# Kernel tuning notes

Hardware: AMD Instinct MI355X
Metric: run time of the kernel (lower is better)

## Reference

```python
import jax, jax.numpy as jnp
import numpy as np

C = 64; H = 80; W = 120; B = 2; V = 3; BV = B * V; D = 20
NEAR = 0.1; FAR = 100.0
BF16 = jnp.bfloat16


def conv2d(x, w, b, pad):
    y = jax.lax.conv_general_dilated(x, w, (1, 1), [(pad, pad), (pad, pad)],
                                     dimension_numbers=('NCHW', 'OIHW', 'NCHW'))
    return y + b[None, :, None, None]


def bn2d(x, g, b, m, v, eps=1e-5):
    # BatchNorm2d in inference mode (running stats)
    scale = g / jnp.sqrt(v + eps)
    return (x - m[None, :, None, None]) * scale[None, :, None, None] + b[None, :, None, None]


def grid_sample(feat, grid):
    # feat [N,C,Hf,Wf], grid [N,Hg,Wg,2] in [-1,1]; bilinear, zeros padding, align_corners=True
    _, _, Hf, Wf = feat.shape
    gx = (grid[..., 0] + 1.0) * 0.5 * (Wf - 1)
    gy = (grid[..., 1] + 1.0) * 0.5 * (Hf - 1)
    x0 = jnp.floor(gx); y0 = jnp.floor(gy)

    def one(f, gx, gy, x0, y0):
        def gather(xi, yi):
            valid = (xi >= 0) & (xi < Wf) & (yi >= 0) & (yi < Hf)
            xc = jnp.clip(xi, 0, Wf - 1).astype(jnp.int32)
            yc = jnp.clip(yi, 0, Hf - 1).astype(jnp.int32)
            return f[:, yc, xc] * valid.astype(f.dtype)
        wx = gx - x0; wy = gy - y0
        return (gather(x0, y0) * ((1 - wx) * (1 - wy))
                + gather(x0 + 1, y0) * (wx * (1 - wy))
                + gather(x0, y0 + 1) * ((1 - wx) * wy)
                + gather(x0 + 1, y0 + 1) * (wx * wy))
    return jax.vmap(one)(feat, gx, gy, x0, y0)


def forward(x, intrinsics, c2ws,
            pf_bn1_g, pf_bn1_b, pf_bn1_m, pf_bn1_v, pf_w1, pf_b1,
            pf_bn2_g, pf_bn2_b, pf_bn2_m, pf_bn2_v, pf_w2, pf_b2,
            cp_w, cp_b, cf_bn_g, cf_bn_b, cf_bn_m, cf_bn_v, cf_w, cf_b):
    # ---- flag[0]: predicted depth -> world xyz, position_fusion ----
    depth = 255.0 * (0.5 * jnp.tanh(x[:, 0]) + 0.5)                       # [BV,H,W]
    d16 = depth.astype(BF16)
    ug = jnp.broadcast_to(jnp.arange(W, dtype=jnp.float32)[None, :], (H, W)).astype(BF16)
    vg = jnp.broadcast_to(jnp.arange(H, dtype=jnp.float32)[:, None], (H, W)).astype(BF16)
    cam = jnp.stack([ug[None] * d16, vg[None] * d16, d16], axis=-1).reshape(BV, H * W, 3)
    Kinv = jnp.linalg.inv(intrinsics.astype(jnp.float32)).astype(BF16)
    xyz = jnp.einsum('nij,npj->npi', Kinv, cam)                           # cam coords
    xyz = jnp.einsum('nij,npj->npi', c2ws[:, :3, :3].astype(BF16), xyz) \
          + c2ws[:, :3, 3].astype(BF16)[:, None, :]                       # world coords
    xyz = xyz.reshape(BV, H, W, 3).transpose(0, 3, 1, 2).astype(x.dtype)
    h = jnp.concatenate([xyz, x], axis=1)                                 # [BV,C+3,H,W]
    h = jax.nn.silu(conv2d(bn2d(h, pf_bn1_g, pf_bn1_b, pf_bn1_m, pf_bn1_v), pf_w1, pf_b1, 4))
    h = jax.nn.silu(conv2d(bn2d(h, pf_bn2_g, pf_bn2_b, pf_bn2_m, pf_bn2_v), pf_w2, pf_b2, 4))

    # ---- flag[1]: multi-view plane-sweep correlation ----
    xr = h.reshape(B, V, C, H, W)
    vb = lambda t: t.transpose(1, 0, 2, 3, 4).reshape(BV, C, H, W)        # 'b v ... -> (v b) ...'
    feat01 = vb(xr)
    Ki = intrinsics.reshape(B, V, 3, 3)
    intr_curr = jax.lax.stop_gradient(
        (Ki * jnp.array([W, H, 1.0], jnp.float32)[None, None, :, None]).transpose(1, 0, 2, 3).reshape(BV, 3, 3))
    E = jax.lax.stop_gradient(c2ws.reshape(B, V, 4, 4))
    Einv = jnp.linalg.inv(E)
    dmin, dmax = 1.0 / FAR, 1.0 / NEAR
    depth_vals = 1.0 / (dmin + jnp.linspace(0.0, 1.0, D) * (dmax - dmin))  # [D]
    pix = jnp.stack([jnp.broadcast_to(jnp.arange(W, dtype=jnp.float32)[None, :], (H, W)),
                     jnp.broadcast_to(jnp.arange(H, dtype=jnp.float32)[:, None], (H, W)),
                     jnp.ones((H, W), jnp.float32)], 0).reshape(3, H * W)
    Kinv_c = jnp.linalg.inv(intr_curr).astype(BF16)

    corr = 0.0
    for idx in range(1, V):
        order = list(range(V))[idx:] + list(range(V))[:idx]
        feat10 = vb(xr[:, jnp.array(order)])                              # [BV,C,H,W]
        pose = jnp.concatenate([E[:, o] @ Einv[:, v0] for v0, o in enumerate(order)], axis=0)  # [BV,4,4]
        pts = jnp.einsum('bij,jp->bip', Kinv_c, pix.astype(BF16))
        pts = jnp.einsum('bij,bjp->bip', pose[:, :3, :3].astype(BF16), pts)
        pts = pts[:, :, None, :] * depth_vals.astype(BF16)[None, None, :, None] \
              + pose[:, :3, 3].astype(BF16)[:, :, None, None]             # [BV,3,D,HW]
        pts = jnp.einsum('bij,bjdp->bidp', intr_curr.astype(BF16), pts).astype(jnp.float32)
        den = jnp.maximum(pts[:, 2], 1e-3)
        grid = jnp.stack([2.0 * pts[:, 0] / den / (W - 1) - 1.0,
                          2.0 * pts[:, 1] / den / (H - 1) - 1.0], axis=-1)
        grid = jax.lax.stop_gradient(grid.reshape(BV, D * H, W, 2))
        warped = grid_sample(feat10, grid).reshape(BV, C, D, H, W)
        corr = corr + jnp.einsum('bchw,bcdhw->bdhw', feat01, warped) / (C ** 0.5)
    corr = corr / (V - 1)

    cin = jnp.concatenate([corr, feat01], axis=1)                         # [BV,D+C,H,W]
    cost = conv2d(cin, cp_w, cp_b, 1).reshape(V, B, C, H, W).transpose(1, 0, 2, 3, 4)
    fused = jnp.concatenate([cost, xr], axis=2).reshape(BV, 2 * C, H, W)
    out = jax.nn.silu(conv2d(bn2d(fused, cf_bn_g, cf_bn_b, cf_bn_m, cf_bn_v), cf_w, cf_b, 4))
    return out


def setup_inputs() -> dict:
    key = jax.random.key(0)
    ks = jax.random.split(key, 24)
    def nrm(i, shape, scale=1.0):
        return scale * jax.random.normal(ks[i], shape, jnp.float32)
    def wconv(i, shape):
        fan_in = int(np.prod(shape[1:]))
        return jax.random.normal(ks[i], shape, jnp.float32) / np.sqrt(fan_in)
    x = nrm(0, (BV, C, H, W))
    Kmat = np.tile(np.array([[1.2, 0, 0.5], [0, 1.6, 0.5], [0, 0, 1.0]], np.float32), (BV, 1, 1))
    intrinsics = jnp.asarray(Kmat)
    c2_list = []
    for i in range(BV):
        th = 0.3 * (i % V) - 0.3
        T = np.eye(4, dtype=np.float32)
        T[:3, :3] = np.array([[np.cos(th), 0, np.sin(th)], [0, 1, 0], [-np.sin(th), 0, np.cos(th)]], np.float32)
        T[:3, 3] = [0.5 * (i % V) - 0.5, 0.0, 0.1]
        c2_list.append(T)
    c2ws = jnp.asarray(np.stack(c2_list))
    # first BN sees raw world-xyz channels (magnitude ~1e4), so realistic running var there
    bn1_v = jnp.concatenate([jnp.full((3,), 1e8, jnp.float32), jnp.ones((C,), jnp.float32)])
    return dict(
        x=x, intrinsics=intrinsics, c2ws=c2ws,
        pf_bn1_g=1.0 + 0.1 * nrm(1, (C + 3,)), pf_bn1_b=0.1 * nrm(2, (C + 3,)),
        pf_bn1_m=0.1 * nrm(3, (C + 3,)), pf_bn1_v=bn1_v,
        pf_w1=wconv(4, (C, C + 3, 9, 9)), pf_b1=0.01 * nrm(5, (C,)),
        pf_bn2_g=1.0 + 0.1 * nrm(6, (C,)), pf_bn2_b=0.1 * nrm(7, (C,)),
        pf_bn2_m=0.1 * nrm(8, (C,)), pf_bn2_v=jnp.ones((C,), jnp.float32),
        pf_w2=wconv(9, (C, C, 9, 9)), pf_b2=0.01 * nrm(10, (C,)),
        cp_w=wconv(11, (C, C + D, 3, 3)), cp_b=0.01 * nrm(12, (C,)),
        cf_bn_g=1.0 + 0.1 * nrm(13, (2 * C,)), cf_bn_b=0.1 * nrm(14, (2 * C,)),
        cf_bn_m=0.1 * nrm(15, (2 * C,)), cf_bn_v=jnp.ones((2 * C,), jnp.float32),
        cf_w=wconv(16, (C, 2 * C, 9, 9)), cf_b=0.01 * nrm(17, (C,)))


def reference(x, intrinsics, c2ws,
              pf_bn1_g, pf_bn1_b, pf_bn1_m, pf_bn1_v, pf_w1, pf_b1,
              pf_bn2_g, pf_bn2_b, pf_bn2_m, pf_bn2_v, pf_w2, pf_b2,
              cp_w, cp_b, cf_bn_g, cf_bn_b, cf_bn_m, cf_bn_v, cf_w, cf_b):
    return forward(x, intrinsics, c2ws,
                   pf_bn1_g, pf_bn1_b, pf_bn1_m, pf_bn1_v, pf_w1, pf_b1,
                   pf_bn2_g, pf_bn2_b, pf_bn2_m, pf_bn2_v, pf_w2, pf_b2,
                   cp_w, cp_b, cf_bn_g, cf_bn_b, cf_bn_m, cf_bn_v, cf_w, cf_b)
```

## Files before the change

### kernel.cpp

```cpp
#include <hip/hip_runtime.h>
#include <math.h>

static constexpr int kH  = 80;
static constexpr int kW  = 120;
static constexpr int kHW = kH * kW;
static constexpr int kBV = 6;
static constexpr int kD  = 20;

typedef __attribute__((ext_vector_type(8)))  short bf16x8;
typedef __attribute__((ext_vector_type(16))) float f32x16;
typedef __attribute__((ext_vector_type(4)))  int   i32x4;
typedef __attribute__((ext_vector_type(2)))  int   i32x2;
typedef __attribute__((ext_vector_type(4)))  float float4v;

__device__ __forceinline__ float bf16r(float x) {
  unsigned u = __float_as_uint(x);
  u += 0x7FFFu + ((u >> 16) & 1u);
  return __uint_as_float(u & 0xFFFF0000u);
}
__device__ __forceinline__ unsigned short bf16c(float x) {
  unsigned u = __float_as_uint(x);
  u += 0x7FFFu + ((u >> 16) & 1u);
  return (unsigned short)(u >> 16);
}
__device__ __forceinline__ int pack2(float a, float b) {
  return (int)((unsigned)bf16c(a) | ((unsigned)bf16c(b) << 16));
}
__device__ __forceinline__ float bl(unsigned pk) {
  return __uint_as_float(pk << 16);
}
__device__ __forceinline__ float bh(unsigned pk) {
  return __uint_as_float(pk & 0xFFFF0000u);
}

struct ConstBuf {
  float bn1_s[67], bn1_o[67];
  float bn2_s[64], bn2_o[64];
  float bnf_s[128], bnf_o[128];
  float Kinv[6][9];
  float Rw[6][9];
  float tw[6][3];
  float Kinvc[6][9];
  float intrc[6][9];
  float poseR[2][6][9];
  float poseT[2][6][3];
  float dvals[20];
};

__device__ void inv3x3(const float* A, float* o) {
  float a = A[0], b = A[1], c = A[2];
  float d = A[3], e = A[4], f = A[5];
  float g = A[6], h = A[7], i = A[8];
  float det = a * (e * i - f * h) - b * (d * i - f * g) + c * (d * h - e * g);
  float id = 1.0f / det;
  o[0] = (e * i - f * h) * id;
  o[1] = -(b * i - c * h) * id;
  o[2] = (b * f - c * e) * id;
  o[3] = -(d * i - f * g) * id;
  o[4] = (a * i - c * g) * id;
  o[5] = -(a * f - c * d) * id;
  o[6] = (d * h - e * g) * id;
  o[7] = -(a * h - b * g) * id;
  o[8] = (a * e - b * d) * id;
}

__device__ void inv4x4(const float* A, float* out) {
  float M[4][8];
  for (int r = 0; r < 4; ++r) {
    for (int c = 0; c < 4; ++c) M[r][c] = A[r * 4 + c];
    for (int c = 0; c < 4; ++c) M[r][4 + c] = (r == c) ? 1.0f : 0.0f;
  }
  for (int col = 0; col < 4; ++col) {
    int p = col;
    float best = fabsf(M[col][col]);
    for (int r = col + 1; r < 4; ++r) {
      float v = fabsf(M[r][col]);
      if (v > best) { best = v; p = r; }
    }
    if (p != col)
      for (int c = 0; c < 8; ++c) { float t = M[col][c]; M[col][c] = M[p][c]; M[p][c] = t; }
    float inv = 1.0f / M[col][col];
    for (int c = 0; c < 8; ++c) M[col][c] *= inv;
    for (int r = 0; r < 4; ++r) {
      if (r == col) continue;
      float f = M[r][col];
      for (int c = 0; c < 8; ++c) M[r][c] -= f * M[col][c];
    }
  }
  for (int r = 0; r < 4; ++r)
    for (int c = 0; c < 4; ++c) out[r * 4 + c] = M[r][4 + c];
}

__device__ void mm4(const float* A, const float* B, float* C) {
  for (int r = 0; r < 4; ++r)
    for (int c = 0; c < 4; ++c) {
      float s = 0.0f;
      for (int k = 0; k < 4; ++k) s += A[r * 4 + k] * B[k * 4 + c];
      C[r * 4 + c] = s;
    }
}

__global__ void consts_kernel(const float* __restrict__ intr, const float* __restrict__ c2,
                              const float* g1, const float* b1, const float* m1, const float* v1,
                              const float* g2, const float* b2, const float* m2, const float* v2,
                              const float* gf, const float* bff, const float* mf, const float* vff,
                              ConstBuf* cb) {
  int tid = threadIdx.x;
  for (int c = tid; c < 67; c += 64) {
    float s = g1[c] / sqrtf(v1[c] + 1e-5f);
    cb->bn1_s[c] = s; cb->bn1_o[c] = b1[c] - m1[c] * s;
  }
  for (int c = tid; c < 64; c += 64) {
    float s = g2[c] / sqrtf(v2[c] + 1e-5f);
    cb->bn2_s[c] = s; cb->bn2_o[c] = b2[c] - m2[c] * s;
  }
  for (int c = tid; c < 128; c += 64) {
    float s = gf[c] / sqrtf(vff[c] + 1e-5f);
    cb->bnf_s[c] = s; cb->bnf_o[c] = bff[c] - mf[c] * s;
  }
  if (tid < 20) {
    float l = (1.0f / 19.0f) * (float)tid;
    cb->dvals[tid] = bf16r(1.0f / (0.01f + l * 9.99f));
  }
  __shared__ float Einv_s[6][16];
  if (tid < 6) {
    float Ki[9];
    inv3x3(intr + tid * 9, Ki);
    for (int k = 0; k < 9; ++k) cb->Kinv[tid][k] = bf16r(Ki[k]);
    const float* T = c2 + tid * 16;
    cb->Rw[tid][0] = bf16r(T[0]);  cb->Rw[tid][1] = bf16r(T[1]);  cb->Rw[tid][2] = bf16r(T[2]);
    cb->Rw[tid][3] = bf16r(T[4]);  cb->Rw[tid][4] = bf16r(T[5]);  cb->Rw[tid][5] = bf16r(T[6]);
    cb->Rw[tid][6] = bf16r(T[8]);  cb->Rw[tid][7] = bf16r(T[9]);  cb->Rw[tid][8] = bf16r(T[10]);
    cb->tw[tid][0] = bf16r(T[3]);  cb->tw[tid][1] = bf16r(T[7]);  cb->tw[tid][2] = bf16r(T[11]);
    inv4x4(T, Einv_s[tid]);
    int vj = tid >> 1, bj = tid & 1, ii = bj * 3 + vj;
    const float* Kk = intr + ii * 9;
    float S[9] = {Kk[0] * 120.0f, Kk[1] * 120.0f, Kk[2] * 120.0f,
                  Kk[3] * 80.0f,  Kk[4] * 80.0f,  Kk[5] * 80.0f,
                  Kk[6],          Kk[7],          Kk[8]};
    for (int k = 0; k < 9; ++k) cb->intrc[tid][k] = bf16r(S[k]);
    float Si[9];
    inv3x3(S, Si);
    for (int k = 0; k < 9; ++k) cb->Kinvc[tid][k] = bf16r(Si[k]);
  }
  __syncthreads();
  if (tid < 12) {
    int t = tid / 6, jj = tid % 6;
    int vj = jj >> 1, bj = jj & 1;
    int o = (vj + t + 1) % 3;
    float P[16];
    mm4(c2 + (bj * 3 + o) * 16, Einv_s[bj * 3 + vj], P);
    for (int r = 0; r < 3; ++r) {
      for (int c = 0; c < 3; ++c) cb->poseR[t][jj][r * 3 + c] = bf16r(P[r * 4 + c]);
      cb->poseT[t][jj][r] = bf16r(P[r * 4 + 3]);
    }
  }
}

template <int K, int CINP, int CINR>
__global__ __launch_bounds__(256)
void prep_w(const float* __restrict__ w, unsigned short* __restrict__ Wp) {
  constexpr int NCH = CINP / 32;
  constexpr int NU = K * K * NCH * 256;
  int u = blockIdx.x * 256 + threadIdx.x;
  if (u >= NU) return;
  int slot = u & 255;
  int rest = u >> 8;
  int ci = rest % NCH;
  int kk = rest / NCH;
  int ky = kk / K, kx = kk - ky * K;
  int oc = slot >> 2;
  int gi = (slot & 3) ^ ((oc >> 2) & 3);
  int chb = ci * 32 + gi * 8;
  unsigned short o[8];
#pragma unroll
  for (int e = 0; e < 8; ++e) {
    int ch = chb + e;
    float val = (ch < CINR) ? w[(((size_t)oc * CINR + ch) * K + ky) * K + kx] : 0.0f;
    o[e] = bf16c(val);
  }
  i32x4 pk;
  pk.x = (int)o[0] | ((int)o[1] << 16);
  pk.y = (int)o[2] | ((int)o[3] << 16);
  pk.z = (int)o[4] | ((int)o[5] << 16);
  pk.w = (int)o[6] | ((int)o[7] << 16);
  *(i32x4*)&Wp[(size_t)u * 8] = pk;
}

__global__ __launch_bounds__(256)
void hn_pack(const float* __restrict__ x, const ConstBuf* __restrict__ cb,
             unsigned short* __restrict__ hn_b) {
  int id = blockIdx.x * 256 + threadIdx.x;
  if (id >= kBV * kHW) return;
  int bv = id / kHW, pix = id - bv * kHW;
  int yy = pix / kW, xx = pix - yy * kW;
  float t0 = tanhf(x[(size_t)bv * 64 * kHW + pix]);
  float depth = 255.0f * (0.5f * t0 + 0.5f);
  float dz = bf16r(depth);
  float cx = bf16r((float)xx * dz);
  float cy = bf16r((float)yy * dz);
  const float* Ki = cb->Kinv[bv];
  float p0 = bf16r(Ki[0] * cx + Ki[1] * cy + Ki[2] * dz);
  float p1 = bf16r(Ki[3] * cx + Ki[4] * cy + Ki[5] * dz);
  float p2 = bf16r(Ki[6] * cx + Ki[7] * cy + Ki[8] * dz);
  const float* R = cb->Rw[bv];
  const float* tw = cb->tw[bv];
  float q[3];
  q[0] = bf16r(bf16r(R[0] * p0 + R[1] * p1 + R[2] * p2) + tw[0]);
  q[1] = bf16r(bf16r(R[3] * p0 + R[4] * p1 + R[5] * p2) + tw[1]);
  q[2] = bf16r(bf16r(R[6] * p0 + R[7] * p1 + R[8] * p2) + tw[2]);
  unsigned short* o = &hn_b[(size_t)id * 96];
  const float* xb = x + (size_t)bv * 64 * kHW + pix;
#pragma unroll
  for (int g = 0; g < 24; ++g) {
    float vv[4];
#pragma unroll
    for (int e = 0; e < 4; ++e) {
      int ch = g * 4 + e;
      float val;
      if (ch < 3) val = q[ch] * cb->bn1_s[ch] + cb->bn1_o[ch];
      else if (ch < 67) val = xb[(size_t)(ch - 3) * kHW] * cb->bn1_s[ch] + cb->bn1_o[ch];
      else val = 0.0f;
      vv[e] = val;
    }
    i32x2 pk = {pack2(vv[0], vv[1]), pack2(vv[2], vv[3])};
    *(i32x2*)(o + g * 4) = pk;
  }
}

template <int CINP, int K, int OUT>
__global__ __launch_bounds__(256)
void conv_mfma(const unsigned short* __restrict__ in_b,
               const unsigned short* __restrict__ Wp,
               const float* __restrict__ bias,
               const ConstBuf* __restrict__ cb,
               float* __restrict__ outf,
               unsigned short* __restrict__ outb,
               unsigned short* __restrict__ outb2) {
  constexpr int NCH = CINP / 32;
  constexpr int KK = K * K;
  constexpr int GN = KK / 3;
  constexpr int PAD = K / 2;
  constexpr int NC = 16 + K - 1;
  constexpr int NR = 16 + K - 1;
  constexpr int NPX = NC * NR;
  __shared__ unsigned short sA[NPX * 32];
  __shared__ unsigned short sB[2][3 * 2048];

  const int tid = threadIdx.x;
  const int w = tid >> 6, l = tid & 63;
  const int bx = blockIdx.x, by = blockIdx.y, bz = blockIdx.z;
  const size_t inbase = (size_t)bz * kHW;

  const int r = l & 31, h = l >> 5;
  const int xloc = r & 15;
  const int rhi = r >> 4;
  f32x16 acc[2][2] = {};

  int boff[2][2];
#pragma unroll
  for (int nt = 0; nt < 2; ++nt)
#pragma unroll
    for (int kc = 0; kc < 2; ++kc) {
      int oc = nt * 32 + (l & 31);
      int gi = kc * 2 + h;
      boff[nt][kc] = (oc * 4 + (gi ^ ((oc >> 2) & 3))) * 8;
    }

  for (int ci = 0; ci < NCH; ++ci) {
    for (int g2 = tid; g2 < NPX * 4; g2 += 256) {
      int px = g2 >> 2, gi = g2 & 3;
      int hy = px / NC, hx = px - hy * NC;
      int gy = by * 16 - PAD + hy, gx = bx * 16 - PAD + hx;
      bool ok = ((unsigned)gy < (unsigned)kH) && ((unsigned)gx < (unsigned)kW);
      i32x4 v = {0, 0, 0, 0};
      if (ok) v = *(const i32x4*)&in_b[(inbase + gy * kW + gx) * CINP + ci * 32 + gi * 8];
      *(i32x4*)&sA[px * 32 + ((gi ^ ((px >> 2) & 3)) << 3)] = v;
    }
#pragma unroll
    for (int t = 0; t < 3; ++t) {
      int u = tid + t * 256;
      int kki = u >> 8, slot = u & 255;
      *(i32x4*)&sB[0][u * 8] =
          *(const i32x4*)&Wp[(((size_t)kki * NCH + ci) * 256 + slot) * 8];
    }
    __syncthreads();

    for (int g = 0; g < GN; ++g) {
      const int cur = g & 1, nxt = cur ^ 1;
      const bool hasnext = (g + 1 < GN);
      i32x4 pf[3];
      if (hasnext) {
#pragma unroll
        for (int t = 0; t < 3; ++t) {
          int u = tid + t * 256;
          int kki = u >> 8, slot = u & 255;
          pf[t] = *(const i32x4*)
              &Wp[(((size_t)((g + 1) * 3 + kki) * NCH + ci) * 256 + slot) * 8];
        }
      }
#pragma unroll
      for (int kki = 0; kki < 3; ++kki) {
        const int kk = g * 3 + kki;
        const int ky = kk / K, kx = kk - ky * K;
        bf16x8 a[2][2];
#pragma unroll
        for (int m = 0; m < 2; ++m) {
          const int hp = (4 * w + 2 * m + rhi + ky) * NC + (xloc + kx);
#pragma unroll
          for (int kc = 0; kc < 2; ++kc) {
            int gi = kc * 2 + h;
            a[m][kc] = *(const bf16x8*)&sA[hp * 32 + ((gi ^ ((hp >> 2) & 3)) << 3)];
          }
        }
        bf16x8 bb[2][2];
#pragma unroll
        for (int nt = 0; nt < 2; ++nt)
#pragma unroll
          for (int kc = 0; kc < 2; ++kc)
            bb[nt][kc] = *(const bf16x8*)&sB[cur][kki * 2048 + boff[nt][kc]];
#pragma unroll
        for (int m = 0; m < 2; ++m)
#pragma unroll
          for (int nt = 0; nt < 2; ++nt) {
            acc[m][nt] = __builtin_amdgcn_mfma_f32_32x32x16_bf16(a[m][0], bb[nt][0], acc[m][nt], 0, 0, 0);
            acc[m][nt] = __builtin_amdgcn_mfma_f32_32x32x16_bf16(a[m][1], bb[nt][1], acc[m][nt], 0, 0, 0);
          }
      }
      if (hasnext) {
#pragma unroll
        for (int t = 0; t < 3; ++t)
          *(i32x4*)&sB[nxt][(tid + t * 256) * 8] = pf[t];
      }
      __syncthreads();
    }
  }

#pragma unroll
  for (int m = 0; m < 2; ++m) {
#pragma unroll
    for (int nt = 0; nt < 2; ++nt) {
      const int oc = nt * 32 + (l & 31);
      const float bs = bias[oc];
      float s2 = 0.f, o2 = 0.f;
      if (OUT == 0) { s2 = cb->bn2_s[oc]; o2 = cb->bn2_o[oc]; }
      if (OUT == 1) { s2 = cb->bnf_s[64 + oc]; o2 = cb->bnf_o[64 + oc]; }
      if (OUT == 2) { s2 = cb->bnf_s[oc]; o2 = cb->bnf_o[oc]; }
#pragma unroll
      for (int reg = 0; reg < 16; ++reg) {
        int row = (reg & 3) + 8 * (reg >> 2) + 4 * h;
        int x = bx * 16 + (row & 15);
        if (x >= kW) continue;
        int y = by * 16 + 4 * w + 2 * m + (row >> 4);
        float v = acc[m][nt][reg] + bs;
        if (OUT != 2) v = v / (1.0f + expf(-v));
        if (OUT == 0) {
          size_t px = inbase + y * kW + x;
          outb[px * 64 + oc] = bf16c(v * s2 + o2);
        } else if (OUT == 1) {
          size_t px = inbase + y * kW + x;
          outb[px * 64 + oc] = bf16c(v);
          outb2[px * 128 + 64 + oc] = bf16c(v * s2 + o2);
        } else if (OUT == 2) {
          int i = (bz & 1) * 3 + (bz >> 1);
          size_t px = (size_t)i * kHW + y * kW + x;
          outb[px * 128 + oc] = bf16c(v * s2 + o2);
        } else {
          outf[((size_t)bz * 64 + oc) * kHW + y * kW + x] = v;
        }
      }
    }
  }
}

__global__ __launch_bounds__(256)
void corr_kernel(const unsigned short* __restrict__ h_b, const ConstBuf* __restrict__ cb,
                 unsigned short* __restrict__ cin_b) {
  __shared__ float sgeo[4][2][40][8];
  const int tid = threadIdx.x;
  const int w = tid >> 6, lane = tid & 63;
  const int pair = blockIdx.x * 4 + w;
  const int j = pair / (kHW / 2);
  const int pix = (pair - j * (kHW / 2)) * 2;
  const int b = j & 1, v = j >> 1;
  const int ph = lane >> 5, cl = lane & 31;
  const int pixl = pix + ph;
  const int dst = b * 3 + v;
  const unsigned f01pk =
      ((const unsigned*)(h_b + ((size_t)dst * kHW + pixl) * 64))[cl];
  const float f01lo = bl(f01pk), f01hi = bh(f01pk);
  const char* sb0 = (const char*)(h_b + (size_t)(b * 3 + ((v + 1) % 3)) * kHW * 64);
  const char* sb1 = (const char*)(h_b + (size_t)(b * 3 + ((v + 2) % 3)) * kHW * 64);

  for (int job = lane; job < 80; job += 64) {
    const int p = job / 40, jj = job - p * 40;
    const int d = jj >> 1, t = jj & 1;
    const int pp = pix + p;
    const int yyp = pp / kW, xxp = pp - yyp * kW;
    const float* Kc = cb->Kinvc[j];
    const float* IC = cb->intrc[j];
    const float uf = (float)xxp, vf = (float)yyp;
    float p1_0 = bf16r(Kc[0] * uf + Kc[1] * vf + Kc[2]);
    float p1_1 = bf16r(Kc[3] * uf + Kc[4] * vf + Kc[5]);
    float p1_2 = bf16r(Kc[6] * uf + Kc[7] * vf + Kc[8]);
    const float* PR = cb->poseR[t][j];
    const float* PT = cb->poseT[t][j];
    float p20 = bf16r(PR[0] * p1_0 + PR[1] * p1_1 + PR[2] * p1_2);
    float p21 = bf16r(PR[3] * p1_0 + PR[4] * p1_1 + PR[5] * p1_2);
    float p22 = bf16r(PR[6] * p1_0 + PR[7] * p1_1 + PR[8] * p1_2);
    float dv = cb->dvals[d];
    float q0 = bf16r(bf16r(p20 * dv) + PT[0]);
    float q1 = bf16r(bf16r(p21 * dv) + PT[1]);
    float q2 = bf16r(bf16r(p22 * dv) + PT[2]);
    float s0 = bf16r(IC[0] * q0 + IC[1] * q1 + IC[2] * q2);
    float s1 = bf16r(IC[3] * q0 + IC[4] * q1 + IC[5] * q2);
    float s2 = bf16r(IC[6] * q0 + IC[7] * q1 + IC[8] * q2);
    float den = fmaxf(s2, 1e-3f);
    float g0 = 2.0f * s0 / den / 119.0f - 1.0f;
    float g1 = 2.0f * s1 / den / 79.0f - 1.0f;
    float gx = (g0 + 1.0f) * 0.5f * 119.0f;
    float gy = (g1 + 1.0f) * 0.5f * 79.0f;
    float x0f = floorf(gx), y0f = floorf(gy);
    float wx = gx - x0f, wy = gy - y0f;
    float x1f = x0f + 1.0f, y1f = y0f + 1.0f;
    float vx0 = (x0f >= 0.0f && x0f < 120.0f) ? 1.0f : 0.0f;
    float vx1 = (x1f >= 0.0f && x1f < 120.0f) ? 1.0f : 0.0f;
    float vy0 = (y0f >= 0.0f && y0f < 80.0f) ? 1.0f : 0.0f;
    float vy1 = (y1f >= 0.0f && y1f < 80.0f) ? 1.0f : 0.0f;
    int xi0 = (int)fminf(fmaxf(x0f, 0.0f), 119.0f);
    int xi1 = (int)fminf(fmaxf(x1f, 0.0f), 119.0f);
    int yi0 = (int)fminf(fmaxf(y0f, 0.0f), 79.0f);
    int yi1 = (int)fminf(fmaxf(y1f, 0.0f), 79.0f);
    int r0b = yi0 * (kW * 128), r1b = yi1 * (kW * 128);
    int c0b = xi0 * 128, c1b = xi1 * 128;
    float* gp = sgeo[w][p][jj];
    gp[0] = __int_as_float(r0b + c0b);
    gp[1] = __int_as_float(r0b + c1b);
    gp[2] = __int_as_float(r1b + c0b);
    gp[3] = __int_as_float(r1b + c1b);
    gp[4] = ((1.0f - wx) * (1.0f - wy)) * (vx0 * vy0);
    gp[5] = (wx * (1.0f - wy)) * (vx1 * vy0);
    gp[6] = ((1.0f - wx) * wy) * (vx0 * vy1);
    gp[7] = (wx * wy) * (vx1 * vy1);
  }
  __syncthreads();

  unsigned short* op = &cin_b[(size_t)(j * kHW + pixl) * 96];
  *(unsigned*)(op + 20 + 2 * cl) = f01pk;
  if (cl < 6) *(unsigned*)(op + 84 + 2 * cl) = 0u;

  const unsigned cl4 = (unsigned)cl * 4u;
#pragma unroll 2
  for (int d = 0; d < kD; ++d) {
    float a = 0.0f;
#pragma unroll
    for (int t = 0; t < 2; ++t) {
      const char* sb = t ? sb1 : sb0;
      const float* gp = sgeo[w][ph][d * 2 + t];
      float4v ga = *(const float4v*)gp;
      float4v gb = *(const float4v*)(gp + 4);
      unsigned k00 = *(const unsigned*)(sb + ((unsigned)__float_as_int(ga.x) + cl4));
      unsigned k10 = *(const unsigned*)(sb + ((unsigned)__float_as_int(ga.y) + cl4));
      unsigned k01 = *(const unsigned*)(sb + ((unsigned)__float_as_int(ga.z) + cl4));
      unsigned k11 = *(const unsigned*)(sb + ((unsigned)__float_as_int(ga.w) + cl4));
      float al = gb.x * bl(k00) + gb.y * bl(k10) + gb.z * bl(k01) + gb.w * bl(k11);
      float ah = gb.x * bh(k00) + gb.y * bh(k10) + gb.z * bh(k01) + gb.w * bh(k11);
      a += al * f01lo + ah * f01hi;
    }
#pragma unroll
    for (int off = 16; off > 0; off >>= 1) a += __shfl_xor(a, off, 64);
    if (cl == 0) op[d] = bf16c(a * 0.0625f);
  }
}

extern "C" void kernel_launch(void* const* d_in, const int* in_sizes, int n_in,
                              void* d_out, int out_size, void* d_ws, size_t ws_size,
                              hipStream_t stream) {
  (void)in_sizes; (void)n_in; (void)out_size; (void)ws_size;
  const float* x    = (const float*)d_in[0];
  const float* intr = (const float*)d_in[1];
  const float* c2w  = (const float*)d_in[2];
  const float* bn1g = (const float*)d_in[3];
  const float* bn1b = (const float*)d_in[4];
  const float* bn1m = (const float*)d_in[5];
  const float* bn1v = (const float*)d_in[6];
  const float* w1   = (const float*)d_in[7];
  const float* b1   = (const float*)d_in[8];
  const float* bn2g = (const float*)d_in[9];
  const float* bn2b = (const float*)d_in[10];
  const float* bn2m = (const float*)d_in[11];
  const float* bn2v = (const float*)d_in[12];
  const float* w2   = (const float*)d_in[13];
  const float* b2   = (const float*)d_in[14];
  const float* cpw  = (const float*)d_in[15];
  const float* cpb  = (const float*)d_in[16];
  const float* bnfg = (const float*)d_in[17];
  const float* bnfb = (const float*)d_in[18];
  const float* bnfm = (const float*)d_in[19];
  const float* bnfv = (const float*)d_in[20];
  const float* wf   = (const float*)d_in[21];
  const float* bff  = (const float*)d_in[22];

  char* ws = (char*)d_ws;
  ConstBuf* cb            = (ConstBuf*)ws;
  unsigned short* hn_b    = (unsigned short*)(ws + 8192);
  unsigned short* h1_b    = (unsigned short*)(ws + 11067392);
  unsigned short* h_b     = (unsigned short*)(ws + 18440192);
  unsigned short* cin_b   = (unsigned short*)(ws + 33185792);
  unsigned short* fused_b = (unsigned short*)(ws + 44244992);
  unsigned short* Wp1     = (unsigned short*)(ws + 58990592);
  unsigned short* Wp2     = (unsigned short*)(ws + 59985920);
  unsigned short* Wpc     = (unsigned short*)(ws + 60649472);
  unsigned short* Wpf     = (unsigned short*)(ws + 60760064);

  consts_kernel<<<1, 64, 0, stream>>>(intr, c2w, bn1g, bn1b, bn1m, bn1v,
                                      bn2g, bn2b, bn2m, bn2v, bnfg, bnfb, bnfm, bnfv, cb);
  prep_w<9, 96, 67><<<243, 256, 0, stream>>>(w1, Wp1);
  prep_w<9, 64, 64><<<162, 256, 0, stream>>>(w2, Wp2);
  prep_w<3, 96, 84><<<27, 256, 0, stream>>>(cpw, Wpc);
  prep_w<9, 128, 128><<<324, 256, 0, stream>>>(wf, Wpf);
  hn_pack<<<225, 256, 0, stream>>>(x, cb, hn_b);

  dim3 cgrid(8, 5, 6);
  conv_mfma<96, 9, 0><<<cgrid, 256, 0, stream>>>(hn_b, Wp1, b1, cb, nullptr, h1_b, nullptr);
  conv_mfma<64, 9, 1><<<cgrid, 256, 0, stream>>>(h1_b, Wp2, b2, cb, nullptr, h_b, fused_b);
  corr_kernel<<<7200, 256, 0, stream>>>(h_b, cb, cin_b);
  conv_mfma<96, 3, 2><<<cgrid, 256, 0, stream>>>(cin_b, Wpc, cpb, cb, nullptr, fused_b, nullptr);
  conv_mfma<128, 9, 3><<<cgrid, 256, 0, stream>>>(fused_b, Wpf, bff, cb, (float*)d_out, nullptr, nullptr);
}
```

Measured before the change: 403.5 us.

## Split conv kernel taps across two wave groups with LDS reduction

The MFMA conv kernel now launches 512 threads: two groups of four waves each take half of the kernel taps (split-K over KK) on the same output tile, then combine partial accumulators through LDS. This doubles the waves per block on a grid of only 240 blocks, meant to raise occupancy and hide latency when there are fewer blocks than compute units can absorb. It costs an extra LDS reduction with syncs, idle waves in the last round when the tap count is odd, and more register pressure under launch bounds of 512.

```diff
diff --git a/kernel.cpp b/kernel.cpp
--- a/kernel.cpp
+++ b/kernel.cpp
@@ -229,7 +229,7 @@
 }
 
 template <int CINP, int K, int OUT>
-__global__ __launch_bounds__(256)
+__global__ __launch_bounds__(512, 2)
 void conv_mfma(const unsigned short* __restrict__ in_b,
                const unsigned short* __restrict__ Wp,
                const float* __restrict__ bias,
@@ -239,22 +239,26 @@
                unsigned short* __restrict__ outb2) {
   constexpr int NCH = CINP / 32;
   constexpr int KK = K * K;
-  constexpr int GN = KK / 3;
+  constexpr int KH0 = (KK + 1) / 2;
+  constexpr int KH1 = KK - KH0;
   constexpr int PAD = K / 2;
   constexpr int NC = 16 + K - 1;
-  constexpr int NR = 16 + K - 1;
-  constexpr int NPX = NC * NR;
+  constexpr int NPX = NC * NC;
   __shared__ unsigned short sA[NPX * 32];
-  __shared__ unsigned short sB[2][3 * 2048];
+  __shared__ unsigned short sB[2][2][2048];
 
   const int tid = threadIdx.x;
   const int w = tid >> 6, l = tid & 63;
+  const int half = w >> 2, mp = w & 3;
+  const int th = tid & 255;
   const int bx = blockIdx.x, by = blockIdx.y, bz = blockIdx.z;
   const size_t inbase = (size_t)bz * kHW;
 
   const int r = l & 31, h = l >> 5;
   const int xloc = r & 15;
   const int rhi = r >> 4;
+  const int kk0 = half ? KH0 : 0;
+  const int myKK = half ? KH1 : KH0;
   f32x16 acc[2][2] = {};
 
   int boff[2][2];
@@ -268,7 +272,7 @@
     }
 
   for (int ci = 0; ci < NCH; ++ci) {
-    for (int g2 = tid; g2 < NPX * 4; g2 += 256) {
+    for (int g2 = tid; g2 < NPX * 4; g2 += 512) {
       int px = g2 >> 2, gi = g2 & 3;
       int hy = px / NC, hx = px - hy * NC;
       int gy = by * 16 - PAD + hy, gx = bx * 16 - PAD + hx;
@@ -277,36 +281,24 @@
       if (ok) v = *(const i32x4*)&in_b[(inbase + gy * kW + gx) * CINP + ci * 32 + gi * 8];
       *(i32x4*)&sA[px * 32 + ((gi ^ ((px >> 2) & 3)) << 3)] = v;
     }
-#pragma unroll
-    for (int t = 0; t < 3; ++t) {
-      int u = tid + t * 256;
-      int kki = u >> 8, slot = u & 255;
-      *(i32x4*)&sB[0][u * 8] =
-          *(const i32x4*)&Wp[(((size_t)kki * NCH + ci) * 256 + slot) * 8];
-    }
+    *(i32x4*)&sB[half][0][th * 8] =
+        *(const i32x4*)&Wp[(((size_t)kk0 * NCH + ci) * 256 + th) * 8];
     __syncthreads();
 
-    for (int g = 0; g < GN; ++g) {
-      const int cur = g & 1, nxt = cur ^ 1;
-      const bool hasnext = (g + 1 < GN);
-      i32x4 pf[3];
-      if (hasnext) {
-#pragma unroll
-        for (int t = 0; t < 3; ++t) {
-          int u = tid + t * 256;
-          int kki = u >> 8, slot = u & 255;
-          pf[t] = *(const i32x4*)
-              &Wp[(((size_t)((g + 1) * 3 + kki) * NCH + ci) * 256 + slot) * 8];
-        }
-      }
-#pragma unroll
-      for (int kki = 0; kki < 3; ++kki) {
-        const int kk = g * 3 + kki;
+    for (int rd = 0; rd < KH0; ++rd) {
+      const int cur = rd & 1, nxt = cur ^ 1;
+      const bool active = rd < myKK;
+      const bool hasnext = (rd + 1) < myKK;
+      i32x4 pf;
+      if (hasnext)
+        pf = *(const i32x4*)&Wp[(((size_t)(kk0 + rd + 1) * NCH + ci) * 256 + th) * 8];
+      if (active) {
+        const int kk = kk0 + rd;
         const int ky = kk / K, kx = kk - ky * K;
         bf16x8 a[2][2];
 #pragma unroll
         for (int m = 0; m < 2; ++m) {
-          const int hp = (4 * w + 2 * m + rhi + ky) * NC + (xloc + kx);
+          const int hp = (4 * mp + 2 * m + rhi + ky) * NC + (xloc + kx);
 #pragma unroll
           for (int kc = 0; kc < 2; ++kc) {
             int gi = kc * 2 + h;
@@ -318,7 +310,7 @@
         for (int nt = 0; nt < 2; ++nt)
 #pragma unroll
           for (int kc = 0; kc < 2; ++kc)
-            bb[nt][kc] = *(const bf16x8*)&sB[cur][kki * 2048 + boff[nt][kc]];
+            bb[nt][kc] = *(const bf16x8*)&sB[half][cur][boff[nt][kc]];
 #pragma unroll
         for (int m = 0; m < 2; ++m)
 #pragma unroll
@@ -327,14 +319,30 @@
             acc[m][nt] = __builtin_amdgcn_mfma_f32_32x32x16_bf16(a[m][1], bb[nt][1], acc[m][nt], 0, 0, 0);
           }
       }
-      if (hasnext) {
-#pragma unroll
-        for (int t = 0; t < 3; ++t)
-          *(i32x4*)&sB[nxt][(tid + t * 256) * 8] = pf[t];
+      if (hasnext) *(i32x4*)&sB[half][nxt][th * 8] = pf;
+      __syncthreads();
+    }
+  }
+
+  float* scratch = (float*)sA;
+#pragma unroll
+  for (int cm = 0; cm < 2; ++cm) {
+#pragma unroll
+    for (int cn = 0; cn < 2; ++cn) {
+      float* sp = scratch + ((mp * 64 + l) * 16);
+      if (half == 1) {
+#pragma unroll
+        for (int q = 0; q < 16; ++q) sp[q] = acc[cm][cn][q];
       }
       __syncthreads();
-    }
-  }
+      if (half == 0) {
+#pragma unroll
+        for (int q = 0; q < 16; ++q) acc[cm][cn][q] += sp[q];
+      }
+      __syncthreads();
+    }
+  }
+  if (half == 1) return;
 
 #pragma unroll
   for (int m = 0; m < 2; ++m) {
@@ -351,7 +359,7 @@
         int row = (reg & 3) + 8 * (reg >> 2) + 4 * h;
         int x = bx * 16 + (row & 15);
         if (x >= kW) continue;
-        int y = by * 16 + 4 * w + 2 * m + (row >> 4);
+        int y = by * 16 + 4 * mp + 2 * m + (row >> 4);
         float v = acc[m][nt][reg] + bs;
         if (OUT != 2) v = v / (1.0f + expf(-v));
         if (OUT == 0) {
@@ -522,9 +530,9 @@
   hn_pack<<<225, 256, 0, stream>>>(x, cb, hn_b);
 
   dim3 cgrid(8, 5, 6);
-  conv_mfma<96, 9, 0><<<cgrid, 256, 0, stream>>>(hn_b, Wp1, b1, cb, nullptr, h1_b, nullptr);
-  conv_mfma<64, 9, 1><<<cgrid, 256, 0, stream>>>(h1_b, Wp2, b2, cb, nullptr, h_b, fused_b);
+  conv_mfma<96, 9, 0><<<cgrid, 512, 0, stream>>>(hn_b, Wp1, b1, cb, nullptr, h1_b, nullptr);
+  conv_mfma<64, 9, 1><<<cgrid, 512, 0, stream>>>(h1_b, Wp2, b2, cb, nullptr, h_b, fused_b);
   corr_kernel<<<7200, 256, 0, stream>>>(h_b, cb, cin_b);
-  conv_mfma<96, 3, 2><<<cgrid, 256, 0, stream>>>(cin_b, Wpc, cpb, cb, nullptr, fused_b, nullptr);
-  conv_mfma<128, 9, 3><<<cgrid, 256, 0, stream>>>(fused_b, Wpf, bff, cb, (float*)d_out, nullptr, nullptr);
-}
+  conv_mfma<96, 3, 2><<<cgrid, 512, 0, stream>>>(cin_b, Wpc, cpb, cb, nullptr, fused_b, nullptr);
+  conv_mfma<128, 9, 3><<<cgrid, 512, 0, stream>>>(fused_b, Wpf, bff, cb, (float*)d_out, nullptr, nullptr);
+}
```

New measurement: 354.4 us. 12.2% less time.
